# Kernel optimization log

Measured on AMD Instinct MI355X. Metric: run time of the kernel, lower is better.

Reference implementation:

```python
import jax, jax.numpy as jnp
import numpy as np

B, NIN, L, N, K, NOUT = 4096, 512, 16, 512, 32, 256
TOTAL = NIN + L * N  # 8704 total nodes in the DAG


def setup_inputs() -> dict:
    key = jax.random.key(0)
    ks = jax.random.split(key, 5)
    x = jax.random.normal(ks[0], (B, NIN), jnp.float32)
    W = jax.random.normal(ks[1], (L, N, K), jnp.float32) * 0.2
    b = jax.random.normal(ks[2], (L, N), jnp.float32) * 0.1
    W_out = jax.random.normal(ks[3], (NOUT, K), jnp.float32) * 0.2
    b_out = jax.random.normal(ks[4], (NOUT,), jnp.float32) * 0.1
    rng = np.random.default_rng(0)
    # layer l may only read nodes computed before it (topological validity)
    idx = np.stack([rng.integers(0, NIN + l * N, size=(N, K)) for l in range(L)]).astype(np.int32)
    idx_out = rng.integers(0, TOTAL, size=(NOUT, K)).astype(np.int32)
    return {"x": x, "W": W, "b": b, "W_out": W_out, "b_out": b_out,
            "idx": jnp.asarray(idx), "idx_out": jnp.asarray(idx_out)}


def reference(x, W, b, W_out, b_out, idx, idx_out):
    # buffer of all node activations, filled topologically (out_dict analog)
    buf0 = jnp.zeros((B, TOTAL), x.dtype).at[:, :NIN].set(x)

    def step(carry, layer):
        buf, l = carry
        li, lW, lb = layer
        gathered = buf[:, li]  # [B, N, K] irregular gather of predecessor outputs
        out = jax.nn.sigmoid(jnp.einsum('bnk,nk->bn', gathered, lW) + lb)  # per-node tiny linear + sigmoid
        buf = jax.lax.dynamic_update_slice(buf, out, (0, NIN + l * N))
        return (buf, l + 1), None

    (buf, _), _ = jax.lax.scan(step, (buf0, jnp.int32(0)), (idx, W, b))
    g = buf[:, idx_out]  # [B, NOUT, K]
    return jax.nn.sigmoid(jnp.einsum('bok,ok->bo', g, W_out) + b_out)
```

## Files before the change

kernel.cpp:

```cpp
#include <hip/hip_runtime.h>
#include <hip/hip_fp16.h>
#include <math.h>

#define B     4096
#define NIN   512
#define L     16
#define N     512
#define K     32
#define NOUT  256
#define TOTAL (NIN + L * N)
#define BROWS 4
#define BLOCK 512

typedef __attribute__((ext_vector_type(4))) _Float16 h4;
typedef __attribute__((ext_vector_type(8))) _Float16 h8;
typedef __attribute__((ext_vector_type(8))) unsigned short u16x8;

__device__ __forceinline__ float sigmoidf_fast(float z) {
    return 1.0f / (1.0f + __expf(-z));
}

__global__ void repack_kernel(const float* __restrict__ W,
                              const int*   __restrict__ idx,
                              const float* __restrict__ W_out,
                              const int*   __restrict__ idx_out,
                              _Float16* __restrict__ wh,
                              unsigned short* __restrict__ i16,
                              _Float16* __restrict__ who,
                              unsigned short* __restrict__ io16)
{
    int g = blockIdx.x * 256 + threadIdx.x;
    if (g < L * N * K) {
        wh[g]  = (_Float16)W[g];
        i16[g] = (unsigned short)idx[g];
    } else {
        int h = g - L * N * K;
        if (h < NOUT * K) {
            who[h]  = (_Float16)W_out[h];
            io16[h] = (unsigned short)idx_out[h];
        }
    }
}

__global__ __launch_bounds__(BLOCK, 4)
void ffnet_kernel(const float* __restrict__ x,
                  const float* __restrict__ b,
                  const float* __restrict__ b_out,
                  const _Float16*       __restrict__ wh,
                  const unsigned short* __restrict__ i16,
                  const _Float16*       __restrict__ who,
                  const unsigned short* __restrict__ io16,
                  float* __restrict__ out)
{
    __shared__ h4 buf[TOTAL];

    const int t  = threadIdx.x;
    const int r0 = blockIdx.x * BROWS;

    {
        h4 v;
        v.x = (_Float16)x[(size_t)(r0 + 0) * NIN + t];
        v.y = (_Float16)x[(size_t)(r0 + 1) * NIN + t];
        v.z = (_Float16)x[(size_t)(r0 + 2) * NIN + t];
        v.w = (_Float16)x[(size_t)(r0 + 3) * NIN + t];
        buf[t] = v;
    }

    u16x8 ni[4];
    {
        const u16x8* ip = (const u16x8*)(i16 + (size_t)t * K);
        ni[0] = ip[0]; ni[1] = ip[1]; ni[2] = ip[2]; ni[3] = ip[3];
    }
    __syncthreads();

#define GATHER8(CI, W8)                                                        \
    {                                                                          \
        _Pragma("unroll")                                                      \
        for (int j = 0; j < 8; ++j) {                                          \
            const int   c = (int)(CI)[j];                                      \
            const float w = (float)(W8)[j];                                    \
            const h4    v = buf[c];                                            \
            acc.x = fmaf((float)v.x, w, acc.x);                                \
            acc.y = fmaf((float)v.y, w, acc.y);                                \
            acc.z = fmaf((float)v.z, w, acc.z);                                \
            acc.w = fmaf((float)v.w, w, acc.w);                                \
        }                                                                      \
    }

    for (int l = 0; l < L; ++l) {
        u16x8 ci[4];
        ci[0] = ni[0]; ci[1] = ni[1]; ci[2] = ni[2]; ci[3] = ni[3];

        const h8* wp = (const h8*)(wh + ((size_t)l * N + t) * K);
        const h8 w0 = wp[0], w1 = wp[1], w2 = wp[2], w3 = wp[3];

        if (l + 1 < L) {
            const u16x8* np = (const u16x8*)(i16 + ((size_t)(l + 1) * N + t) * K);
            ni[0] = np[0]; ni[1] = np[1]; ni[2] = np[2]; ni[3] = np[3];
        }

        float4 acc = make_float4(0.f, 0.f, 0.f, 0.f);
        GATHER8(ci[0], w0)
        GATHER8(ci[1], w1)
        GATHER8(ci[2], w2)
        GATHER8(ci[3], w3)

        const float bb = b[l * N + t];
        h4 o;
        o.x = (_Float16)sigmoidf_fast(acc.x + bb);
        o.y = (_Float16)sigmoidf_fast(acc.y + bb);
        o.z = (_Float16)sigmoidf_fast(acc.z + bb);
        o.w = (_Float16)sigmoidf_fast(acc.w + bb);
        buf[NIN + l * N + t] = o;
        __syncthreads();
    }

    if (t < NOUT) {
        const u16x8* ip = (const u16x8*)(io16 + (size_t)t * K);
        const h8*    wp = (const h8*)   (who  + (size_t)t * K);
        const u16x8 i0 = ip[0], i1 = ip[1], i2 = ip[2], i3 = ip[3];
        const h8    w0 = wp[0], w1 = wp[1], w2 = wp[2], w3 = wp[3];

        float4 acc = make_float4(0.f, 0.f, 0.f, 0.f);
        GATHER8(i0, w0)
        GATHER8(i1, w1)
        GATHER8(i2, w2)
        GATHER8(i3, w3)

        const float bb = b_out[t];
        out[(size_t)(r0 + 0) * NOUT + t] = sigmoidf_fast(acc.x + bb);
        out[(size_t)(r0 + 1) * NOUT + t] = sigmoidf_fast(acc.y + bb);
        out[(size_t)(r0 + 2) * NOUT + t] = sigmoidf_fast(acc.z + bb);
        out[(size_t)(r0 + 3) * NOUT + t] = sigmoidf_fast(acc.w + bb);
    }
#undef GATHER8
}

extern "C" void kernel_launch(void* const* d_in, const int* in_sizes, int n_in,
                              void* d_out, int out_size, void* d_ws, size_t ws_size,
                              hipStream_t stream) {
    const float* x     = (const float*)d_in[0];
    const float* W     = (const float*)d_in[1];
    const float* b     = (const float*)d_in[2];
    const float* W_out = (const float*)d_in[3];
    const float* b_out = (const float*)d_in[4];
    const int*   idx   = (const int*)d_in[5];
    const int*   idx_o = (const int*)d_in[6];
    float* out = (float*)d_out;

    char* ws = (char*)d_ws;
    _Float16*       wh   = (_Float16*)      (ws);
    unsigned short* i16  = (unsigned short*)(ws + 524288);
    _Float16*       who  = (_Float16*)      (ws + 1048576);
    unsigned short* io16 = (unsigned short*)(ws + 1048576 + 16384);

    const int total_pack = L * N * K + NOUT * K;
    repack_kernel<<<dim3((total_pack + 255) / 256), dim3(256), 0, stream>>>(
        W, idx, W_out, idx_o, wh, i16, who, io16);

    ffnet_kernel<<<dim3(B / BROWS), dim3(BLOCK), 0, stream>>>(
        x, b, b_out, wh, i16, who, io16, out);
}
```

Before: 158.9 us.

## Pack fp16 FMAs, reorder per-neuron indices to spread LDS banks, unroll layer pairs

The per-neuron repack now counting-sorts each neuron's 32 predecessor indices by their low 4 bits and rotates the result by neuron id. The aim is that lanes reading in lockstep hit different LDS banks, so gather conflicts drop. Inside the gather, accumulation switches to packed fp16 FMAs over groups of 8, which are promoted to fp32 once per group. This roughly halves the VALU work, at some cost in accumulation precision. The layer loop is unrolled by two with double-buffered index prefetch, and the last prefetch loads the output-layer indices.

```diff
diff --git a/kernel.cpp b/kernel.cpp
--- a/kernel.cpp
+++ b/kernel.cpp
@@ -8,13 +8,16 @@
 #define N     512
 #define K     32
 #define NOUT  256
+#define HID   (L * N)
 #define TOTAL (NIN + L * N)
 #define BROWS 4
 #define BLOCK 512
 
-typedef __attribute__((ext_vector_type(4))) _Float16 h4;
+typedef __attribute__((ext_vector_type(2))) _Float16 hv2;
 typedef __attribute__((ext_vector_type(8))) _Float16 h8;
 typedef __attribute__((ext_vector_type(8))) unsigned short u16x8;
+
+struct alignas(8) hh { hv2 lo, hi; };
 
 __device__ __forceinline__ float sigmoidf_fast(float z) {
     return 1.0f / (1.0f + __expf(-z));
@@ -29,111 +32,158 @@
                               _Float16* __restrict__ who,
                               unsigned short* __restrict__ io16)
 {
-    int g = blockIdx.x * 256 + threadIdx.x;
-    if (g < L * N * K) {
-        wh[g]  = (_Float16)W[g];
-        i16[g] = (unsigned short)idx[g];
+    const int n = blockIdx.x * 256 + threadIdx.x;
+    const int* ip; const float* wp; _Float16* wo; unsigned short* io;
+    if (n < HID) {
+        ip = idx + (size_t)n * K;      wp = W + (size_t)n * K;
+        wo = wh + (size_t)n * K;       io = i16 + (size_t)n * K;
+    } else if (n < HID + NOUT) {
+        const int m = n - HID;
+        ip = idx_out + (size_t)m * K;  wp = W_out + (size_t)m * K;
+        wo = who + (size_t)m * K;      io = io16 + (size_t)m * K;
     } else {
-        int h = g - L * N * K;
-        if (h < NOUT * K) {
-            who[h]  = (_Float16)W_out[h];
-            io16[h] = (unsigned short)idx_out[h];
-        }
-    }
-}
+        return;
+    }
+    const int rot = n & 31;
+
+    int ci[K]; float cw[K];
+#pragma unroll
+    for (int j = 0; j < K; ++j) { ci[j] = ip[j]; cw[j] = wp[j]; }
+
+    unsigned long long h0 = 0, h1 = 0;
+#pragma unroll
+    for (int j = 0; j < K; ++j) {
+        const int key = ci[j] & 15;
+        const unsigned long long one = 1ull << ((key & 7) << 3);
+        if (key < 8) h0 += one; else h1 += one;
+    }
+    unsigned long long o0 = 0, o1 = 0;
+    {
+        unsigned run = 0;
+#pragma unroll
+        for (int kk = 0; kk < 8; ++kk) {
+            o0 |= (unsigned long long)run << (kk << 3);
+            run += (unsigned)((h0 >> (kk << 3)) & 0xffull);
+        }
+#pragma unroll
+        for (int kk = 0; kk < 8; ++kk) {
+            o1 |= (unsigned long long)run << (kk << 3);
+            run += (unsigned)((h1 >> (kk << 3)) & 0xffull);
+        }
+    }
+#pragma unroll
+    for (int j = 0; j < K; ++j) {
+        const int key = ci[j] & 15;
+        const int sh  = (key & 7) << 3;
+        int pos;
+        if (key < 8) { pos = (int)((o0 >> sh) & 0xff); o0 += 1ull << sh; }
+        else         { pos = (int)((o1 >> sh) & 0xff); o1 += 1ull << sh; }
+        const int slot = (pos + rot) & 31;
+        io[slot] = (unsigned short)ci[j];
+        wo[slot] = (_Float16)cw[j];
+    }
+}
+
+#define GROUP8(CI, W8, ACC)                                                   \
+    {                                                                         \
+        hv2 aL = {(_Float16)0.f, (_Float16)0.f};                              \
+        hv2 aH = {(_Float16)0.f, (_Float16)0.f};                              \
+        _Pragma("unroll")                                                     \
+        for (int j = 0; j < 8; ++j) {                                         \
+            const int c = (int)(CI)[j];                                       \
+            const hh  v = buf[c];                                             \
+            hv2 wt2; wt2.x = (W8)[j]; wt2.y = (W8)[j];                        \
+            aL = __builtin_elementwise_fma(v.lo, wt2, aL);                    \
+            aH = __builtin_elementwise_fma(v.hi, wt2, aH);                    \
+        }                                                                     \
+        ACC.x += (float)aL.x;  ACC.y += (float)aL.y;                          \
+        ACC.z += (float)aH.x;  ACC.w += (float)aH.y;                          \
+    }
+
+#define LAYER(IDXQ, LI)                                                       \
+    {                                                                         \
+        const h8* wp = (const h8*)(wh + ((size_t)(LI) * N + t) * K);          \
+        const h8 w0 = wp[0], w1 = wp[1], w2 = wp[2], w3 = wp[3];              \
+        float4 acc = make_float4(0.f, 0.f, 0.f, 0.f);                         \
+        GROUP8(IDXQ[0], w0, acc)                                              \
+        GROUP8(IDXQ[1], w1, acc)                                              \
+        GROUP8(IDXQ[2], w2, acc)                                              \
+        GROUP8(IDXQ[3], w3, acc)                                              \
+        const float bb = bias[(LI) * N + t];                                  \
+        hh o;                                                                 \
+        o.lo.x = (_Float16)sigmoidf_fast(acc.x + bb);                         \
+        o.lo.y = (_Float16)sigmoidf_fast(acc.y + bb);                         \
+        o.hi.x = (_Float16)sigmoidf_fast(acc.z + bb);                         \
+        o.hi.y = (_Float16)sigmoidf_fast(acc.w + bb);                         \
+        buf[NIN + (LI) * N + t] = o;                                          \
+    }
 
 __global__ __launch_bounds__(BLOCK, 4)
 void ffnet_kernel(const float* __restrict__ x,
-                  const float* __restrict__ b,
-                  const float* __restrict__ b_out,
+                  const float* __restrict__ bias,
+                  const float* __restrict__ bias_out,
                   const _Float16*       __restrict__ wh,
                   const unsigned short* __restrict__ i16,
                   const _Float16*       __restrict__ who,
                   const unsigned short* __restrict__ io16,
                   float* __restrict__ out)
 {
-    __shared__ h4 buf[TOTAL];
+    __shared__ hh buf[TOTAL];
 
     const int t  = threadIdx.x;
     const int r0 = blockIdx.x * BROWS;
 
     {
-        h4 v;
-        v.x = (_Float16)x[(size_t)(r0 + 0) * NIN + t];
-        v.y = (_Float16)x[(size_t)(r0 + 1) * NIN + t];
-        v.z = (_Float16)x[(size_t)(r0 + 2) * NIN + t];
-        v.w = (_Float16)x[(size_t)(r0 + 3) * NIN + t];
+        hh v;
+        v.lo.x = (_Float16)x[(size_t)(r0 + 0) * NIN + t];
+        v.lo.y = (_Float16)x[(size_t)(r0 + 1) * NIN + t];
+        v.hi.x = (_Float16)x[(size_t)(r0 + 2) * NIN + t];
+        v.hi.y = (_Float16)x[(size_t)(r0 + 3) * NIN + t];
         buf[t] = v;
     }
 
-    u16x8 ni[4];
+    u16x8 ia[4], ib[4];
     {
         const u16x8* ip = (const u16x8*)(i16 + (size_t)t * K);
-        ni[0] = ip[0]; ni[1] = ip[1]; ni[2] = ip[2]; ni[3] = ip[3];
+        ia[0] = ip[0]; ia[1] = ip[1]; ia[2] = ip[2]; ia[3] = ip[3];
     }
     __syncthreads();
 
-#define GATHER8(CI, W8)                                                        \
-    {                                                                          \
-        _Pragma("unroll")                                                      \
-        for (int j = 0; j < 8; ++j) {                                          \
-            const int   c = (int)(CI)[j];                                      \
-            const float w = (float)(W8)[j];                                    \
-            const h4    v = buf[c];                                            \
-            acc.x = fmaf((float)v.x, w, acc.x);                                \
-            acc.y = fmaf((float)v.y, w, acc.y);                                \
-            acc.z = fmaf((float)v.z, w, acc.z);                                \
-            acc.w = fmaf((float)v.w, w, acc.w);                                \
-        }                                                                      \
-    }
-
-    for (int l = 0; l < L; ++l) {
-        u16x8 ci[4];
-        ci[0] = ni[0]; ci[1] = ni[1]; ci[2] = ni[2]; ci[3] = ni[3];
-
-        const h8* wp = (const h8*)(wh + ((size_t)l * N + t) * K);
+    for (int l = 0; l < L; l += 2) {
+        {
+            const u16x8* np = (const u16x8*)(i16 + ((size_t)(l + 1) * N + t) * K);
+            ib[0] = np[0]; ib[1] = np[1]; ib[2] = np[2]; ib[3] = np[3];
+        }
+        LAYER(ia, l)
+        __syncthreads();
+
+        if (l + 2 < L) {
+            const u16x8* np = (const u16x8*)(i16 + ((size_t)(l + 2) * N + t) * K);
+            ia[0] = np[0]; ia[1] = np[1]; ia[2] = np[2]; ia[3] = np[3];
+        } else if (t < NOUT) {
+            const u16x8* np = (const u16x8*)(io16 + (size_t)t * K);
+            ia[0] = np[0]; ia[1] = np[1]; ia[2] = np[2]; ia[3] = np[3];
+        }
+        LAYER(ib, l + 1)
+        __syncthreads();
+    }
+
+    if (t < NOUT) {
+        const h8* wp = (const h8*)(who + (size_t)t * K);
         const h8 w0 = wp[0], w1 = wp[1], w2 = wp[2], w3 = wp[3];
 
-        if (l + 1 < L) {
-            const u16x8* np = (const u16x8*)(i16 + ((size_t)(l + 1) * N + t) * K);
-            ni[0] = np[0]; ni[1] = np[1]; ni[2] = np[2]; ni[3] = np[3];
-        }
-
         float4 acc = make_float4(0.f, 0.f, 0.f, 0.f);
-        GATHER8(ci[0], w0)
-        GATHER8(ci[1], w1)
-        GATHER8(ci[2], w2)
-        GATHER8(ci[3], w3)
-
-        const float bb = b[l * N + t];
-        h4 o;
-        o.x = (_Float16)sigmoidf_fast(acc.x + bb);
-        o.y = (_Float16)sigmoidf_fast(acc.y + bb);
-        o.z = (_Float16)sigmoidf_fast(acc.z + bb);
-        o.w = (_Float16)sigmoidf_fast(acc.w + bb);
-        buf[NIN + l * N + t] = o;
-        __syncthreads();
-    }
-
-    if (t < NOUT) {
-        const u16x8* ip = (const u16x8*)(io16 + (size_t)t * K);
-        const h8*    wp = (const h8*)   (who  + (size_t)t * K);
-        const u16x8 i0 = ip[0], i1 = ip[1], i2 = ip[2], i3 = ip[3];
-        const h8    w0 = wp[0], w1 = wp[1], w2 = wp[2], w3 = wp[3];
-
-        float4 acc = make_float4(0.f, 0.f, 0.f, 0.f);
-        GATHER8(i0, w0)
-        GATHER8(i1, w1)
-        GATHER8(i2, w2)
-        GATHER8(i3, w3)
-
-        const float bb = b_out[t];
+        GROUP8(ia[0], w0, acc)
+        GROUP8(ia[1], w1, acc)
+        GROUP8(ia[2], w2, acc)
+        GROUP8(ia[3], w3, acc)
+
+        const float bb = bias_out[t];
         out[(size_t)(r0 + 0) * NOUT + t] = sigmoidf_fast(acc.x + bb);
         out[(size_t)(r0 + 1) * NOUT + t] = sigmoidf_fast(acc.y + bb);
         out[(size_t)(r0 + 2) * NOUT + t] = sigmoidf_fast(acc.z + bb);
         out[(size_t)(r0 + 3) * NOUT + t] = sigmoidf_fast(acc.w + bb);
     }
-#undef GATHER8
 }
 
 extern "C" void kernel_launch(void* const* d_in, const int* in_sizes, int n_in,
@@ -154,8 +204,8 @@
     _Float16*       who  = (_Float16*)      (ws + 1048576);
     unsigned short* io16 = (unsigned short*)(ws + 1048576 + 16384);
 
-    const int total_pack = L * N * K + NOUT * K;
-    repack_kernel<<<dim3((total_pack + 255) / 256), dim3(256), 0, stream>>>(
+    const int nneur = HID + NOUT;
+    repack_kernel<<<dim3((nneur + 255) / 256), dim3(256), 0, stream>>>(
         W, idx, W_out, idx_o, wh, i16, who, io16);
 
     ffnet_kernel<<<dim3(B / BROWS), dim3(BLOCK), 0, stream>>>(
```

Measured after the change: 164.4 us. 1.03x slower.
